# Kernel tuning notes

Measured on AMD Instinct MI355X. Metric: run time of the kernel, lower is better.

Reference implementation:

```python
import jax, jax.numpy as jnp
import numpy as np

N_NODES = 100000
N_EDGES = 1600000
HEADS = 8
CH = 16
NEG_SLOPE = 0.2


def setup_inputs() -> dict:
    key = jax.random.key(0)
    ks = jax.random.split(key, 8)
    x = jax.random.normal(ks[0], (N_NODES, 16), dtype=jnp.float32)
    edge_index = jax.random.randint(ks[1], (2, N_EDGES), 0, N_NODES, dtype=jnp.int64)
    W = jax.random.normal(ks[2], (16, HEADS * CH), dtype=jnp.float32) * 0.25
    att_src = jax.random.normal(ks[3], (HEADS, CH), dtype=jnp.float32) * 0.25
    att_dst = jax.random.normal(ks[4], (HEADS, CH), dtype=jnp.float32) * 0.25
    bias = jax.random.normal(ks[5], (HEADS * CH,), dtype=jnp.float32) * 0.1
    fc_w = jax.random.normal(ks[6], (HEADS * CH, 5), dtype=jnp.float32) * 0.1
    fc_b = jax.random.normal(ks[7], (5,), dtype=jnp.float32) * 0.1
    return {"x": x, "edge_index": edge_index, "W": W, "att_src": att_src,
            "att_dst": att_dst, "bias": bias, "fc_w": fc_w, "fc_b": fc_b}


def reference(x, edge_index, W, att_src, att_dst, bias, fc_w, fc_b):
    N = x.shape[0]
    # PyG GATConv default: add self loops
    loops = jnp.arange(N, dtype=edge_index.dtype)
    src = jnp.concatenate([edge_index[0], loops])
    dst = jnp.concatenate([edge_index[1], loops])

    h = (x @ W).reshape(N, HEADS, CH)                 # [N,H,C]
    a_src = jnp.einsum('nhc,hc->nh', h, att_src)      # [N,H]
    a_dst = jnp.einsum('nhc,hc->nh', h, att_dst)      # [N,H]

    e = a_src[src] + a_dst[dst]                       # [E,H]
    e = jax.nn.leaky_relu(e, NEG_SLOPE)
    # segment softmax over edges grouped by destination node
    e_max = jax.ops.segment_max(e, dst, num_segments=N)
    e_exp = jnp.exp(e - e_max[dst])
    denom = jax.ops.segment_sum(e_exp, dst, num_segments=N)
    alpha = e_exp / (denom[dst] + 1e-16)              # [E,H]

    msg = alpha[:, :, None] * h[src]                  # [E,H,C]
    out = jax.ops.segment_sum(msg, dst, num_segments=N)  # [N,H,C]
    out = out.reshape(N, HEADS * CH) + bias           # concat heads + bias

    out = jax.nn.relu(out)
    # dropout is identity in eval mode
    logits = out @ fc_w + fc_b                        # [N,5]
    return jax.nn.log_softmax(logits, axis=1)
```

## Files before the change

kernel.cpp:

```cpp
#include <hip/hip_runtime.h>
#include <hip/hip_bf16.h>
#include <hip/hip_fp16.h>
#include <math.h>

#define N_NODES 100000
#define N_EDGES 1600000
#define HEADS 8
#define HC 128
#define LOG2E 1.44269504f

#define DPB 64
#define NB 1563
#define NBP (NB + 1)
#define NCH 512
#define EPC (N_EDGES / NCH)
#define CAPS 1664
#define WSTR (CAPS + 4)
#define NA 196

__global__ __launch_bounds__(512) void k_prep(
    const float* __restrict__ x, const float* __restrict__ W,
    const float* __restrict__ att_s, const float* __restrict__ att_d,
    const int* __restrict__ ei,
    unsigned short* __restrict__ a_srcb, float* __restrict__ a_dst,
    uint4* __restrict__ x2b,
    int* __restrict__ offs, unsigned* __restrict__ stg) {
    __shared__ int smem[2048 + EPC];
    __shared__ int ws8[8];
    int t = threadIdx.x;
    if (blockIdx.x >= NCH) {
        float* sM = (float*)smem;
        if (t < 256) {
            int k = t >> 4, h2 = t & 15;
            const float* av = (h2 < 8) ? att_s : att_d;
            int h = h2 & 7;
            float s = 0.f;
#pragma unroll
            for (int c = 0; c < 16; ++c)
                s = fmaf(W[k * HC + h * 16 + c], av[h * 16 + c], s);
            sM[k * 16 + h2] = s * LOG2E;
        }
        __syncthreads();
        int node = (blockIdx.x - NCH) * 512 + t;
        if (node < N_NODES) {
            const float4* xr = (const float4*)(x + node * 16);
            float4 x0 = xr[0], x1 = xr[1], x2 = xr[2], x3 = xr[3];
            float xv[16] = {x0.x, x0.y, x0.z, x0.w, x1.x, x1.y, x1.z, x1.w,
                            x2.x, x2.y, x2.z, x2.w, x3.x, x3.y, x3.z, x3.w};
            union { uint4 u[2]; __hip_bfloat162 b[8]; } px;
#pragma unroll
            for (int k = 0; k < 8; ++k)
                px.b[k] = __float22bfloat162_rn(float2{xv[2 * k], xv[2 * k + 1]});
            x2b[node * 2] = px.u[0];
            x2b[node * 2 + 1] = px.u[1];
            float oo[16];
#pragma unroll
            for (int h2 = 0; h2 < 16; ++h2) {
                float o = 0.f;
#pragma unroll
                for (int k = 0; k < 16; ++k) o = fmaf(xv[k], sM[k * 16 + h2], o);
                oo[h2] = o;
            }
            union { uint4 u; unsigned short s[8]; } pb;
#pragma unroll
            for (int h = 0; h < 8; ++h)
                pb.s[h] = __bfloat16_as_ushort(__float2bfloat16(oo[h]));
            *(uint4*)(a_srcb + (size_t)node * 8) = pb.u;
            float4 d0 = {oo[8], oo[9], oo[10], oo[11]};
            float4 d1 = {oo[12], oo[13], oo[14], oo[15]};
            *(float4*)(a_dst + (size_t)node * 8) = d0;
            *(float4*)(a_dst + (size_t)node * 8 + 4) = d1;
        }
    } else {
        int* hist = smem;
        unsigned* entries = (unsigned*)(smem + 2048);
        int c = blockIdx.x;
        hist[t] = 0; hist[t + 512] = 0; hist[t + 1024] = 0; hist[t + 1536] = 0;
        __syncthreads();
        int beg = c * EPC, end = beg + EPC;
        for (int e = beg + t; e < end; e += 512)
            atomicAdd(&hist[ei[N_EDGES + e] >> 6], 1);
        __syncthreads();
        int i0 = 4 * t;
        int v0 = hist[i0], v1 = hist[i0 + 1], v2 = hist[i0 + 2], v3 = hist[i0 + 3];
        int s1 = v0 + v1, s2 = s1 + v2, T = s2 + v3;
        int lane = t & 63, wv = t >> 6;
        int inc = T;
#pragma unroll
        for (int off = 1; off < 64; off <<= 1) {
            int y = __shfl_up(inc, off);
            if (lane >= off) inc += y;
        }
        if (lane == 63) ws8[wv] = inc;
        __syncthreads();
        int wbase = 0;
        for (int k = 0; k < wv; ++k) wbase += ws8[k];
        int e0 = wbase + inc - T;
        hist[i0] = e0; hist[i0 + 1] = e0 + v0;
        hist[i0 + 2] = e0 + s1; hist[i0 + 3] = e0 + s2;
        __syncthreads();
        int row = c * NBP;
        for (int b = t; b < NB; b += 512) offs[row + b] = hist[b];
        if (t == 0) offs[row + NB] = EPC;
        __syncthreads();
        for (int e = beg + t; e < end; e += 512) {
            int src = ei[e], dst = ei[N_EDGES + e];
            int pos = atomicAdd(&hist[dst >> 6], 1);
            entries[pos] = ((unsigned)(dst & 63) << 17) | (unsigned)src;
        }
        __syncthreads();
        unsigned* so = stg + beg;
        for (int i = t; i < EPC; i += 512) so[i] = entries[i];
    }
}

__global__ __launch_bounds__(256) void k_tr(const int* __restrict__ offs,
                                            int* __restrict__ offsT) {
    __shared__ int tile[64][65];
    int b0 = (blockIdx.x >> 3) * 64;
    int c0 = (blockIdx.x & 7) * 64;
    int t = threadIdx.x;
    for (int i = t; i < 4096; i += 256) {
        int cc = i >> 6, bb = i & 63;
        int b = b0 + bb;
        tile[bb][cc] = (b < NBP) ? offs[(c0 + cc) * NBP + b] : 0;
    }
    __syncthreads();
    for (int i = t; i < 4096; i += 256) {
        int bb = i >> 6, cc = i & 63;
        int b = b0 + bb;
        if (b < NBP) offsT[b * NCH + c0 + cc] = tile[bb][cc];
    }
}

__global__ __launch_bounds__(512) void k_gather(
    const __hip_bfloat162* __restrict__ x2b,
    const unsigned short* __restrict__ a_srcb, const float* __restrict__ W,
    const float* __restrict__ a_dst,
    const int* __restrict__ offsT, const unsigned* __restrict__ stg,
    const float* __restrict__ bias, const float* __restrict__ fc_w,
    const float* __restrict__ fc_b, float* __restrict__ out) {
    __shared__ __align__(16) unsigned buf0[(8 * WSTR) / 2];
    __shared__ __align__(16) int sbuf[CAPS];
    __shared__ __align__(16) float sW[16 * HC];
    __shared__ __align__(16) float sad[8 * DPB + 8];
    __shared__ int hist[DPB];
    __shared__ int bs[DPB + 1];
    __shared__ int rord[DPB];
    __shared__ int ws8[8];
    unsigned* estage = buf0;
    unsigned short* wst = (unsigned short*)buf0;
    int* cstage = sbuf;
    int* o0_s = sbuf;
    int* myb_s = sbuf + 512;
    int b = blockIdx.x, t = threadIdx.x;
    int d0 = b * DPB;
    for (int i = t; i < 16 * HC; i += 512) {
        int c = i & 127, k = i >> 7;
        int blk = c >> 3;
        int sb = blk ^ ((blk >> 2) & 3);
        sW[k * HC + sb * 8 + (c & 7)] = W[i];
    }
    sad[t] = (d0 * 8 + t < N_NODES * 8) ? a_dst[(size_t)d0 * 8 + t] : 0.f;
    if (t < 8) sad[8 * DPB + t] = -100000.f;
    int lane = t & 63, wv = t >> 6;
    {
        int o0 = offsT[b * NCH + t];
        int len = offsT[(b + 1) * NCH + t] - o0;
        o0_s[t] = o0;
        int inc = len;
#pragma unroll
        for (int off = 1; off < 64; off <<= 1) {
            int y = __shfl_up(inc, off);
            if (lane >= off) inc += y;
        }
        if (lane == 63) ws8[wv] = inc;
        __syncthreads();
        int wbase = 0;
        for (int k = 0; k < wv; ++k) wbase += ws8[k];
        myb_s[t] = wbase + inc - len;
        if (t == 511) myb_s[NCH] = wbase + inc;
    }
    if (t < DPB) hist[t] = (d0 + t < N_NODES) ? 1 : 0;
    __syncthreads();
    int tot = myb_s[NCH];
    for (int i = t; i < tot; i += 512) {
        int lo = 0, hi = NCH - 1;
#pragma unroll
        for (int s = 0; s < 9; ++s) {
            int mid = (lo + hi + 1) >> 1;
            if (myb_s[mid] <= i) lo = mid; else hi = mid - 1;
        }
        estage[i] = stg[lo * EPC + o0_s[lo] + (i - myb_s[lo])];
    }
    __syncthreads();
    for (int i = t; i < tot; i += 512) atomicAdd(&hist[estage[i] >> 17], 1);
    __syncthreads();
    if (t < 64) {
        int gd = d0 + t;
        bool val = gd < N_NODES;
        int len = hist[t];
        int plen = (len + 3) & ~3;
        int iv = plen;
#pragma unroll
        for (int off = 1; off < 64; off <<= 1) {
            int y = __shfl_up(iv, off);
            if (t >= off) iv += y;
        }
        int excl = iv - plen;
        bs[t] = excl;
        if (t == 63) bs[64] = iv;
        if (val) cstage[excl] = (t << 17) | gd;
        hist[t] = excl + (val ? 1 : 0);
        for (int k = len; k < plen; ++k) cstage[excl + k] = (64 << 17);
        int key = (plen << 6) | t;
#pragma unroll
        for (int k = 2; k <= 64; k <<= 1) {
#pragma unroll
            for (int jj = k >> 1; jj >= 1; jj >>= 1) {
                int partner = __shfl_xor(key, jj);
                bool up = ((t & k) == 0);
                bool takeMax = (((t & jj) != 0) == up);
                key = takeMax ? (key > partner ? key : partner)
                              : (key < partner ? key : partner);
            }
        }
        rord[t] = key & 63;
    }
    __syncthreads();
    for (int i = t; i < tot; i += 512) {
        unsigned u = estage[i];
        int pos = atomicAdd(&hist[u >> 17], 1);
        cstage[pos] = (int)u;
    }
    __syncthreads();
    int ctot = bs[DPB];
    for (int i = t; i < ctot; i += 512) {
        unsigned u = (unsigned)cstage[i];
        int s = (int)(u & 0x1FFFF);
        int dl = (int)(u >> 17);
        union { uint4 v; __hip_bfloat162 b2[4]; } pa;
        pa.v = *(const uint4*)(a_srcb + (size_t)s * 8);
        const float* adp = sad + dl * 8;
        float4 ad0 = *(const float4*)(adp);
        float4 ad1 = *(const float4*)(adp + 4);
        float2 s01 = __bfloat1622float2(pa.b2[0]);
        float2 s23 = __bfloat1622float2(pa.b2[1]);
        float2 s45 = __bfloat1622float2(pa.b2[2]);
        float2 s67 = __bfloat1622float2(pa.b2[3]);
        float e[8] = {s01.x + ad0.x, s01.y + ad0.y, s23.x + ad0.z, s23.y + ad0.w,
                      s45.x + ad1.x, s45.y + ad1.y, s67.x + ad1.z, s67.y + ad1.w};
#pragma unroll
        for (int h = 0; h < 8; ++h) {
            float eh = fmaxf(e[h], 0.2f * e[h]);
            float w = exp2f(eh);
            wst[h * WSTR + i] = __half_as_ushort(__float2half(w));
        }
    }
    __syncthreads();
    int q = t & 15, g = t >> 4;
    int head = q >> 1, i8 = q & 1;
    int c0 = head * 16 + i8 * 8;
    int blk0 = c0 >> 3;
    int sw0 = (blk0 ^ ((blk0 >> 2) & 3)) * 8;
    const unsigned short* wrow = wst + head * WSTR;
    int xofs = i8 * 16;
    const char* xb = (const char*)x2b;
    float bb[8], fwv[8][5], fbv[5];
#pragma unroll
    for (int m = 0; m < 8; ++m) bb[m] = bias[c0 + m];
#pragma unroll
    for (int m = 0; m < 8; ++m)
#pragma unroll
        for (int jj = 0; jj < 5; ++jj) fwv[m][jj] = fc_w[(c0 + m) * 5 + jj];
#pragma unroll
    for (int jj = 0; jj < 5; ++jj) fbv[jj] = fc_b[jj];
    for (int l4 = 0; l4 < 2; ++l4) {
        int l = rord[l4 == 0 ? g : 63 - g];
        int gd = d0 + l;
        if (gd >= N_NODES) continue;
        int beg = bs[l], end = bs[l + 1];
        float A[8] = {0.f, 0.f, 0.f, 0.f, 0.f, 0.f, 0.f, 0.f};
        float wsum = 0.f;
        auto acc = [&](const uint4& xv, float w) {
            union { uint4 v; __hip_bfloat162 b2[4]; } xx; xx.v = xv;
            float2 f0 = __bfloat1622float2(xx.b2[0]);
            float2 f1 = __bfloat1622float2(xx.b2[1]);
            float2 f2 = __bfloat1622float2(xx.b2[2]);
            float2 f3 = __bfloat1622float2(xx.b2[3]);
            A[0] = fmaf(w, f0.x, A[0]); A[1] = fmaf(w, f0.y, A[1]);
            A[2] = fmaf(w, f1.x, A[2]); A[3] = fmaf(w, f1.y, A[3]);
            A[4] = fmaf(w, f2.x, A[4]); A[5] = fmaf(w, f2.y, A[5]);
            A[6] = fmaf(w, f3.x, A[6]); A[7] = fmaf(w, f3.y, A[7]);
        };
        for (int j = beg; j < end; j += 4) {
            int4 cs = *(const int4*)(cstage + j);
            uint2 wu = *(const uint2*)(wrow + j);
            union { uint2 u2; __half2 h2[2]; } wq; wq.u2 = wu;
            float2 w01 = __half22float2(wq.h2[0]);
            float2 w23 = __half22float2(wq.h2[1]);
            int s0 = cs.x & 0x1FFFF, s1 = cs.y & 0x1FFFF;
            int s2 = cs.z & 0x1FFFF, s3 = cs.w & 0x1FFFF;
            uint4 xv0 = *(const uint4*)(xb + ((s0 << 5) + xofs));
            uint4 xv1 = *(const uint4*)(xb + ((s1 << 5) + xofs));
            uint4 xv2 = *(const uint4*)(xb + ((s2 << 5) + xofs));
            uint4 xv3 = *(const uint4*)(xb + ((s3 << 5) + xofs));
            acc(xv0, w01.x); acc(xv1, w01.y);
            acc(xv2, w23.x); acc(xv3, w23.y);
            wsum += (w01.x + w01.y) + (w23.x + w23.y);
        }
        float inv = 1.f / (wsum + 1e-16f);
#pragma unroll
        for (int m = 0; m < 8; ++m) A[m] *= inv;
        float ov[8] = {0.f, 0.f, 0.f, 0.f, 0.f, 0.f, 0.f, 0.f};
#pragma unroll
        for (int m = 0; m < 8; ++m) {
            float a = A[m];
            float ap = __shfl_xor(A[m], 1);
            const float* w0r = sW + (i8 * 8 + m) * HC + sw0;
            const float* w1r = sW + ((1 - i8) * 8 + m) * HC + sw0;
#pragma unroll
            for (int o = 0; o < 8; ++o) ov[o] = fmaf(a, w0r[o], ov[o]);
#pragma unroll
            for (int o = 0; o < 8; ++o) ov[o] = fmaf(ap, w1r[o], ov[o]);
        }
#pragma unroll
        for (int m = 0; m < 8; ++m) ov[m] = fmaxf(ov[m] + bb[m], 0.f);
        float p[5];
#pragma unroll
        for (int jj = 0; jj < 5; ++jj) {
            float sacc = 0.f;
#pragma unroll
            for (int m = 0; m < 8; ++m) sacc = fmaf(ov[m], fwv[m][jj], sacc);
            p[jj] = sacc;
        }
#pragma unroll
        for (int off = 8; off >= 1; off >>= 1)
#pragma unroll
            for (int jj = 0; jj < 5; ++jj) p[jj] += __shfl_xor(p[jj], off);
        if (q == 0) {
            float lg[5], mx = -1e30f;
#pragma unroll
            for (int jj = 0; jj < 5; ++jj) {
                lg[jj] = p[jj] + fbv[jj];
                mx = fmaxf(mx, lg[jj]);
            }
            float sum = 0.f;
#pragma unroll
            for (int jj = 0; jj < 5; ++jj) sum += __expf(lg[jj] - mx);
            float ls = mx + __logf(sum);
#pragma unroll
            for (int jj = 0; jj < 5; ++jj) out[gd * 5 + jj] = lg[jj] - ls;
        }
    }
}

extern "C" void kernel_launch(void* const* d_in, const int* in_sizes, int n_in,
                              void* d_out, int out_size, void* d_ws, size_t ws_size,
                              hipStream_t stream) {
    const float* x     = (const float*)d_in[0];
    const int*   ei    = (const int*)d_in[1];
    const float* W     = (const float*)d_in[2];
    const float* att_s = (const float*)d_in[3];
    const float* att_d = (const float*)d_in[4];
    const float* bias  = (const float*)d_in[5];
    const float* fc_w  = (const float*)d_in[6];
    const float* fc_b  = (const float*)d_in[7];
    float* out = (float*)d_out;

    char* ws = (char*)d_ws;
    size_t off = 0;
    auto carve = [&](size_t bytes) {
        void* p = ws + off;
        off = (off + bytes + 255) & ~(size_t)255;
        return p;
    };
    unsigned short* a_srcb = (unsigned short*)carve((size_t)N_NODES * HEADS * 2);
    float*    a_dst = (float*)   carve((size_t)N_NODES * HEADS * 4);
    uint4*    x2b   = (uint4*)   carve((size_t)N_NODES * 32);
    int*      offs  = (int*)     carve((size_t)NCH * NBP * 4);
    int*      offsT = (int*)     carve((size_t)NBP * NCH * 4);
    unsigned* stg   = (unsigned*)carve((size_t)N_EDGES * 4);

    k_prep<<<NCH + NA, 512, 0, stream>>>(x, W, att_s, att_d, ei,
                                         a_srcb, a_dst, x2b, offs, stg);
    k_tr<<<200, 256, 0, stream>>>(offs, offsT);
    k_gather<<<NB, 512, 0, stream>>>((const __hip_bfloat162*)x2b, a_srcb, W,
                                     a_dst, offsT, stg, bias, fc_w, fc_b, out);
}
```

Baseline: 169.2 us.

## Drop offset transpose kernel, fuse histogram into gather, remove degree sort

Removes the separate transpose kernel and has the gather kernel read per-chunk offsets directly with a strided access. The per-destination histogram atomics are folded into the edge staging loop, saving a barrier and a second pass. The bitonic sort that balanced destinations across thread groups by degree is replaced with a fixed pairing. This saves a kernel launch and some per-block sync work, at the cost of uncoalesced offset reads and possible load imbalance.

Result: faster. 162.4 us, median of 2 (-4.0%).

```diff
diff --git a/kernel.cpp b/kernel.cpp
--- a/kernel.cpp
+++ b/kernel.cpp
@@ -114,30 +114,11 @@
     }
 }
 
-__global__ __launch_bounds__(256) void k_tr(const int* __restrict__ offs,
-                                            int* __restrict__ offsT) {
-    __shared__ int tile[64][65];
-    int b0 = (blockIdx.x >> 3) * 64;
-    int c0 = (blockIdx.x & 7) * 64;
-    int t = threadIdx.x;
-    for (int i = t; i < 4096; i += 256) {
-        int cc = i >> 6, bb = i & 63;
-        int b = b0 + bb;
-        tile[bb][cc] = (b < NBP) ? offs[(c0 + cc) * NBP + b] : 0;
-    }
-    __syncthreads();
-    for (int i = t; i < 4096; i += 256) {
-        int bb = i >> 6, cc = i & 63;
-        int b = b0 + bb;
-        if (b < NBP) offsT[b * NCH + c0 + cc] = tile[bb][cc];
-    }
-}
-
 __global__ __launch_bounds__(512) void k_gather(
     const __hip_bfloat162* __restrict__ x2b,
     const unsigned short* __restrict__ a_srcb, const float* __restrict__ W,
     const float* __restrict__ a_dst,
-    const int* __restrict__ offsT, const unsigned* __restrict__ stg,
+    const int* __restrict__ offs, const unsigned* __restrict__ stg,
     const float* __restrict__ bias, const float* __restrict__ fc_w,
     const float* __restrict__ fc_b, float* __restrict__ out) {
     __shared__ __align__(16) unsigned buf0[(8 * WSTR) / 2];
@@ -146,7 +127,6 @@
     __shared__ __align__(16) float sad[8 * DPB + 8];
     __shared__ int hist[DPB];
     __shared__ int bs[DPB + 1];
-    __shared__ int rord[DPB];
     __shared__ int ws8[8];
     unsigned* estage = buf0;
     unsigned short* wst = (unsigned short*)buf0;
@@ -165,8 +145,8 @@
     if (t < 8) sad[8 * DPB + t] = -100000.f;
     int lane = t & 63, wv = t >> 6;
     {
-        int o0 = offsT[b * NCH + t];
-        int len = offsT[(b + 1) * NCH + t] - o0;
+        int o0 = offs[t * NBP + b];
+        int len = offs[t * NBP + b + 1] - o0;
         o0_s[t] = o0;
         int inc = len;
 #pragma unroll
@@ -191,10 +171,10 @@
             int mid = (lo + hi + 1) >> 1;
             if (myb_s[mid] <= i) lo = mid; else hi = mid - 1;
         }
-        estage[i] = stg[lo * EPC + o0_s[lo] + (i - myb_s[lo])];
-    }
-    __syncthreads();
-    for (int i = t; i < tot; i += 512) atomicAdd(&hist[estage[i] >> 17], 1);
+        unsigned u = stg[lo * EPC + o0_s[lo] + (i - myb_s[lo])];
+        estage[i] = u;
+        atomicAdd(&hist[u >> 17], 1);
+    }
     __syncthreads();
     if (t < 64) {
         int gd = d0 + t;
@@ -213,19 +193,6 @@
         if (val) cstage[excl] = (t << 17) | gd;
         hist[t] = excl + (val ? 1 : 0);
         for (int k = len; k < plen; ++k) cstage[excl + k] = (64 << 17);
-        int key = (plen << 6) | t;
-#pragma unroll
-        for (int k = 2; k <= 64; k <<= 1) {
-#pragma unroll
-            for (int jj = k >> 1; jj >= 1; jj >>= 1) {
-                int partner = __shfl_xor(key, jj);
-                bool up = ((t & k) == 0);
-                bool takeMax = (((t & jj) != 0) == up);
-                key = takeMax ? (key > partner ? key : partner)
-                              : (key < partner ? key : partner);
-            }
-        }
-        rord[t] = key & 63;
     }
     __syncthreads();
     for (int i = t; i < tot; i += 512) {
@@ -276,9 +243,9 @@
 #pragma unroll
     for (int jj = 0; jj < 5; ++jj) fbv[jj] = fc_b[jj];
     for (int l4 = 0; l4 < 2; ++l4) {
-        int l = rord[l4 == 0 ? g : 63 - g];
+        int l = g * 2 + l4;
         int gd = d0 + l;
-        if (gd >= N_NODES) continue;
+        if (gd >= N_NODES) break;
         int beg = bs[l], end = bs[l + 1];
         float A[8] = {0.f, 0.f, 0.f, 0.f, 0.f, 0.f, 0.f, 0.f};
         float wsum = 0.f;
@@ -379,12 +346,10 @@
     float*    a_dst = (float*)   carve((size_t)N_NODES * HEADS * 4);
     uint4*    x2b   = (uint4*)   carve((size_t)N_NODES * 32);
     int*      offs  = (int*)     carve((size_t)NCH * NBP * 4);
-    int*      offsT = (int*)     carve((size_t)NBP * NCH * 4);
     unsigned* stg   = (unsigned*)carve((size_t)N_EDGES * 4);
 
     k_prep<<<NCH + NA, 512, 0, stream>>>(x, W, att_s, att_d, ei,
                                          a_srcb, a_dst, x2b, offs, stg);
-    k_tr<<<200, 256, 0, stream>>>(offs, offsT);
     k_gather<<<NB, 512, 0, stream>>>((const __hip_bfloat162*)x2b, a_srcb, W,
-                                     a_dst, offsT, stg, bias, fc_w, fc_b, out);
+                                     a_dst, offs, stg, bias, fc_w, fc_b, out);
 }
```
